# Optimization experiments

Measured on AMD Instinct MI355X. Metric: run time of the kernel, lower is better.

The kernel has to match this reference:

```python
import jax, jax.numpy as jnp
import numpy as np

EMB = 128
HEADS = 8
B = 8
T = 2048


def setup_inputs() -> dict:
    key = jax.random.key(0)
    ks = jax.random.split(key, 6)
    x = jax.random.normal(ks[0], (B, T, EMB), dtype=jnp.float32)
    # torch Linear(emb, heads*emb, bias=False): store as (in, out) so y = x @ W
    scale = 1.0 / np.sqrt(EMB)
    Wq = jax.random.uniform(ks[1], (EMB, HEADS * EMB), jnp.float32, -scale, scale)
    Wk = jax.random.uniform(ks[2], (EMB, HEADS * EMB), jnp.float32, -scale, scale)
    Wv = jax.random.uniform(ks[3], (EMB, HEADS * EMB), jnp.float32, -scale, scale)
    so = 1.0 / np.sqrt(HEADS * EMB)
    Wo = jax.random.uniform(ks[4], (HEADS * EMB, EMB), jnp.float32, -so, so)
    bo = jax.random.uniform(ks[5], (EMB,), jnp.float32, -so, so)
    return {"x": x, "Wq": Wq, "Wk": Wk, "Wv": Wv, "Wo": Wo, "bo": bo}


def reference(x, Wq, Wk, Wv, Wo, bo):
    b, t, e = x.shape
    h = HEADS
    q = (x @ Wq).reshape(b, t, h, e)  # [b,t,h,e]
    k = (x @ Wk).reshape(b, t, h, e)
    v = (x @ Wv).reshape(b, t, h, e)
    # scores: [b,h,q,k], scaled by sqrt(e) (per-head dim == emb here)
    scores = jnp.einsum('bqhe,bkhe->bhqk', q, k) / jnp.sqrt(jnp.asarray(e, x.dtype))
    attn = jax.nn.softmax(scores, axis=-1)
    out = jnp.einsum('bhqk,bkhe->bqhe', attn, v).reshape(b, t, h * e)
    return out @ Wo + bo
```

## Files before the change

### kernel.cpp

```cpp
#include <hip/hip_runtime.h>

using bf16x8 = __attribute__((ext_vector_type(8))) short;
using f32x4  = __attribute__((ext_vector_type(4))) float;

__device__ __forceinline__ ushort f2bf(float f) {
    union { float f; unsigned int u; } c; c.f = f;
    unsigned int u = c.u;
    u = (u + 0x7fffu + ((u >> 16) & 1u)) >> 16;
    return (ushort)u;
}

__device__ __forceinline__ void dma16(const ushort* g, ushort* l) {
    __builtin_amdgcn_global_load_lds(
        (const __attribute__((address_space(1))) unsigned int*)g,
        (__attribute__((address_space(3))) unsigned int*)l, 16, 0, 0);
}

constexpr int BB   = 8;
constexpr int HH   = 8;
constexpr int TT   = 2048;
constexpr int DD   = 128;
#define C2F (0.08838834764831845f * 1.4426950408889634f)

__global__ void prep_kernel(const float* __restrict__ x,
                            const float* __restrict__ Wq, const float* __restrict__ Wk,
                            const float* __restrict__ Wv, const float* __restrict__ Wo,
                            ushort* __restrict__ xb, ushort* __restrict__ WqkvT,
                            ushort* __restrict__ WoT) {
    int t = blockIdx.x * 256 + threadIdx.x;
    if (t < 524288) {
        float4 v = ((const float4*)x)[t];
        ushort4 o;
        o.x = f2bf(v.x); o.y = f2bf(v.y); o.z = f2bf(v.z); o.w = f2bf(v.w);
        ((ushort4*)xb)[t] = o;
    } else if (t < 524288 + 393216) {
        int i = t - 524288;
        int j = i >> 7, kk = i & 127;
        const float* W = (j < 1024) ? Wq : ((j < 2048) ? Wk : Wv);
        int jj = j & 1023;
        WqkvT[j * 128 + kk] = f2bf(W[kk * 1024 + jj]);
    } else {
        int i = t - 917504;
        int e = i >> 10, kk = i & 1023;
        WoT[e * 1024 + kk] = f2bf(Wo[kk * 128 + e]);
    }
}

__global__ __launch_bounds__(256, 2)
void qkv_gemm(const ushort* __restrict__ xb, const ushort* __restrict__ WqkvT,
              ushort* __restrict__ q, ushort* __restrict__ k, ushort* __restrict__ vt) {
    __shared__ ushort Al[128 * 136];
    __shared__ ushort Bl[128 * 136];
    const int tid = threadIdx.x;
    const int n0 = blockIdx.x * 128, m0 = blockIdx.y * 128;

    for (int s = tid; s < 2048; s += 256) {
        int row = s >> 4, oct = s & 15;
        *(uint4*)&Al[row * 136 + oct * 8] = *(const uint4*)&xb[m0 * 128 + s * 8];
        *(uint4*)&Bl[row * 136 + oct * 8] = *(const uint4*)&WqkvT[n0 * 128 + s * 8];
    }
    __syncthreads();

    const int w = tid >> 6, lane = tid & 63, l15 = lane & 15, g = lane >> 4;
    const int wm = (w & 1) * 64, wn = (w >> 1) * 64;
    f32x4 acc[4][4] = {};

#pragma unroll
    for (int ks = 0; ks < 4; ks++) {
        bf16x8 af[4], bfr[4];
#pragma unroll
        for (int mb = 0; mb < 4; mb++)
            af[mb] = *(const bf16x8*)&Al[(wm + mb * 16 + l15) * 136 + ks * 32 + g * 8];
#pragma unroll
        for (int nb = 0; nb < 4; nb++)
            bfr[nb] = *(const bf16x8*)&Bl[(wn + nb * 16 + l15) * 136 + ks * 32 + g * 8];
#pragma unroll
        for (int mb = 0; mb < 4; mb++)
#pragma unroll
            for (int nb = 0; nb < 4; nb++)
                acc[mb][nb] = __builtin_amdgcn_mfma_f32_16x16x32_bf16(af[mb], bfr[nb], acc[mb][nb], 0, 0, 0);
    }

    const int which = n0 >> 10;
    const int b = m0 >> 11;
    const int h = (n0 >> 7) & 7;
    const int bh = b * HH + h;
    if (which == 0) {
#pragma unroll
        for (int mb = 0; mb < 4; mb++)
#pragma unroll
            for (int nb = 0; nb < 4; nb++)
#pragma unroll
                for (int r = 0; r < 4; r++) {
                    int t = (m0 + wm + mb * 16 + g * 4 + r) & 2047;
                    int e = wn + nb * 16 + l15;
                    q[((size_t)bh * TT + t) * DD + e] = f2bf(acc[mb][nb][r]);
                }
    } else if (which == 1) {
#pragma unroll
        for (int mb = 0; mb < 4; mb++)
#pragma unroll
            for (int nb = 0; nb < 4; nb++)
#pragma unroll
                for (int r = 0; r < 4; r++) {
                    int t = (m0 + wm + mb * 16 + g * 4 + r) & 2047;
                    int e = wn + nb * 16 + l15;
                    int esw = ((((e >> 3) ^ (t & 7)) << 3) | (e & 7));
                    k[((size_t)bh * TT + t) * DD + esw] = f2bf(acc[mb][nb][r]);
                }
    } else {
        __syncthreads();
        ushort* Tl = Al;
#pragma unroll
        for (int mb = 0; mb < 4; mb++)
#pragma unroll
            for (int nb = 0; nb < 4; nb++)
#pragma unroll
                for (int r = 0; r < 4; r++)
                    Tl[(wn + nb * 16 + l15) * 136 + wm + mb * 16 + g * 4 + r] = f2bf(acc[mb][nb][r]);
        __syncthreads();
        const int c0 = (m0 & 2047) >> 6;
        for (int s = tid; s < 2048; s += 256) {
            int e = s >> 4, x = s & 15;
            int c = c0 + (x >> 3), pos = x & 7;
            int tsrc = ((pos ^ (e & 7)) * 8) + (x >> 3) * 64;
            uint4 val = *(const uint4*)&Tl[e * 136 + tsrc];
            *(uint4*)&vt[(size_t)(((bh * 32 + c) * 128) + e) * 64 + pos * 8] = val;
        }
    }
}

__global__ __launch_bounds__(256, 2)
void attn_kernel(const ushort* __restrict__ q, const ushort* __restrict__ k,
                 const ushort* __restrict__ vt, ushort* __restrict__ ao) {
    __shared__ ushort Kl[2][64 * 128];
    __shared__ ushort Vl[2][128 * 64];
    __shared__ ushort Pl[4 * 32 * 64];

    const int idx = blockIdx.x;
    const int qt128 = idx & 15, h = (idx >> 4) & 7, b = idx >> 7;
    const int t0 = qt128 * 128;
    const int bh = b * HH + h;
    const ushort* qg  = q  + (size_t)bh * TT * DD;
    const ushort* kg  = k  + (size_t)bh * TT * DD;
    const ushort* vtg = vt + (size_t)bh * 32 * DD * 64;

    const int tid = threadIdx.x, w = tid >> 6, lane = tid & 63;
    const int l15 = lane & 15, g = lane >> 4;
    const int sw = l15 & 7;

    bf16x8 qf[2][4];
#pragma unroll
    for (int qt = 0; qt < 2; qt++)
#pragma unroll
        for (int ks = 0; ks < 4; ks++)
            qf[qt][ks] = *(const bf16x8*)&qg[(size_t)(t0 + w * 32 + qt * 16 + l15) * DD + ks * 32 + g * 8];

    {
        const int seg0 = w * 2048 + lane * 8;
#pragma unroll
        for (int i = 0; i < 4; i++) {
            int seg = seg0 + i * 512;
            dma16(kg  + seg, &Kl[0][seg]);
            dma16(vtg + seg, &Vl[0][seg]);
        }
    }

    f32x4 o[2][8] = {};
    float ls[2] = {0.0f, 0.0f};

    for (int c = 0; c < 32; c++) {
        const int cur = c & 1;
        __syncthreads();

        if (c < 31) {
            const ushort* kn = kg  + (size_t)(c + 1) * 8192;
            const ushort* vn = vtg + (size_t)(c + 1) * 8192;
            const int seg0 = w * 2048 + lane * 8;
#pragma unroll
            for (int i = 0; i < 4; i++) {
                int seg = seg0 + i * 512;
                dma16(kn + seg, &Kl[cur ^ 1][seg]);
                dma16(vn + seg, &Vl[cur ^ 1][seg]);
            }
        }

        f32x4 st[4][2] = {};
#pragma unroll
        for (int kt = 0; kt < 4; kt++)
#pragma unroll
            for (int ks = 0; ks < 4; ks++) {
                bf16x8 kf = *(const bf16x8*)&Kl[cur][(kt * 16 + l15) * 128 + (((ks * 4 + g) ^ sw) * 8)];
                st[kt][0] = __builtin_amdgcn_mfma_f32_16x16x32_bf16(kf, qf[0][ks], st[kt][0], 0, 0, 0);
                st[kt][1] = __builtin_amdgcn_mfma_f32_16x16x32_bf16(kf, qf[1][ks], st[kt][1], 0, 0, 0);
            }

#pragma unroll
        for (int qt = 0; qt < 2; qt++) {
            float ps = 0.0f;
#pragma unroll
            for (int kt = 0; kt < 4; kt++) {
                ushort4 pk;
                float p0 = __builtin_amdgcn_exp2f(st[kt][qt][0] * C2F);
                float p1 = __builtin_amdgcn_exp2f(st[kt][qt][1] * C2F);
                float p2 = __builtin_amdgcn_exp2f(st[kt][qt][2] * C2F);
                float p3 = __builtin_amdgcn_exp2f(st[kt][qt][3] * C2F);
                ps += (p0 + p1) + (p2 + p3);
                pk.x = f2bf(p0); pk.y = f2bf(p1); pk.z = f2bf(p2); pk.w = f2bf(p3);
                int kb = 2 * kt + (g >> 1);
                *(ushort4*)&Pl[w * 2048 + (qt * 16 + l15) * 64 + ((kb ^ sw) * 8) + (g & 1) * 4] = pk;
            }
            ls[qt] += ps;
        }

#pragma unroll
        for (int ns = 0; ns < 2; ns++) {
            int rb = ((ns * 4 + g) ^ sw) * 8;
            bf16x8 pa0 = *(const bf16x8*)&Pl[w * 2048 + (l15) * 64 + rb];
            bf16x8 pa1 = *(const bf16x8*)&Pl[w * 2048 + (16 + l15) * 64 + rb];
#pragma unroll
            for (int eb = 0; eb < 8; eb++) {
                bf16x8 vb = *(const bf16x8*)&Vl[cur][(eb * 16 + l15) * 64 + rb];
                o[0][eb] = __builtin_amdgcn_mfma_f32_16x16x32_bf16(pa0, vb, o[0][eb], 0, 0, 0);
                o[1][eb] = __builtin_amdgcn_mfma_f32_16x16x32_bf16(pa1, vb, o[1][eb], 0, 0, 0);
            }
        }
    }

#pragma unroll
    for (int qt = 0; qt < 2; qt++) {
        float tot = ls[qt];
        tot += __shfl_xor(tot, 16);
        tot += __shfl_xor(tot, 32);
        float inv[4];
#pragma unroll
        for (int r = 0; r < 4; r++)
            inv[r] = 1.0f / __shfl(tot, g * 4 + r, 64);
#pragma unroll
        for (int eb = 0; eb < 8; eb++)
#pragma unroll
            for (int r = 0; r < 4; r++) {
                int m = t0 + w * 32 + qt * 16 + g * 4 + r;
                int col = h * 128 + eb * 16 + l15;
                ao[(size_t)(b * TT + m) * 1024 + col] = f2bf(o[qt][eb][r] * inv[r]);
            }
    }
}

__global__ __launch_bounds__(256, 2)
void outproj_gemm(const ushort* __restrict__ ao, const ushort* __restrict__ WoT,
                  const float* __restrict__ bo, float* __restrict__ out) {
    __shared__ ushort Al[64 * 72];
    __shared__ ushort Bl[64 * 72];
    const int tid = threadIdx.x;
    const int n0 = blockIdx.x * 64, m0 = blockIdx.y * 64;
    const int w = tid >> 6, lane = tid & 63, l15 = lane & 15, g = lane >> 4;
    const int wm = (w & 1) * 32, wn = (w >> 1) * 32;
    f32x4 acc[2][2] = {};

    for (int kc = 0; kc < 16; kc++) {
        int k0 = kc * 64;
        __syncthreads();
        for (int s = tid; s < 512; s += 256) {
            int row = s >> 3, oct = s & 7;
            *(uint4*)&Al[row * 72 + oct * 8] = *(const uint4*)&ao[(size_t)(m0 + row) * 1024 + k0 + oct * 8];
            *(uint4*)&Bl[row * 72 + oct * 8] = *(const uint4*)&WoT[(n0 + row) * 1024 + k0 + oct * 8];
        }
        __syncthreads();
#pragma unroll
        for (int ks = 0; ks < 2; ks++) {
            bf16x8 af[2], bfr[2];
#pragma unroll
            for (int mb = 0; mb < 2; mb++)
                af[mb] = *(const bf16x8*)&Al[(wm + mb * 16 + l15) * 72 + ks * 32 + g * 8];
#pragma unroll
            for (int nb = 0; nb < 2; nb++)
                bfr[nb] = *(const bf16x8*)&Bl[(wn + nb * 16 + l15) * 72 + ks * 32 + g * 8];
#pragma unroll
            for (int mb = 0; mb < 2; mb++)
#pragma unroll
                for (int nb = 0; nb < 2; nb++)
                    acc[mb][nb] = __builtin_amdgcn_mfma_f32_16x16x32_bf16(af[mb], bfr[nb], acc[mb][nb], 0, 0, 0);
        }
    }

#pragma unroll
    for (int mb = 0; mb < 2; mb++)
#pragma unroll
        for (int nb = 0; nb < 2; nb++) {
            int j = n0 + wn + nb * 16 + l15;
            float bias = bo[j];
#pragma unroll
            for (int r = 0; r < 4; r++) {
                int m = m0 + wm + mb * 16 + g * 4 + r;
                out[(size_t)m * 128 + j] = acc[mb][nb][r] + bias;
            }
        }
}

extern "C" void kernel_launch(void* const* d_in, const int* in_sizes, int n_in,
                              void* d_out, int out_size, void* d_ws, size_t ws_size,
                              hipStream_t stream) {
    const float* x  = (const float*)d_in[0];
    const float* Wq = (const float*)d_in[1];
    const float* Wk = (const float*)d_in[2];
    const float* Wv = (const float*)d_in[3];
    const float* Wo = (const float*)d_in[4];
    const float* bo = (const float*)d_in[5];
    float* out = (float*)d_out;

    char* ws = (char*)d_ws;
    ushort* xb    = (ushort*)(ws);
    ushort* WqkvT = (ushort*)(ws + 4194304);
    ushort* WoT   = (ushort*)(ws + 4980736);
    ushort* qb    = (ushort*)(ws + 5242880);
    ushort* kb    = (ushort*)(ws + 38797312);
    ushort* vtb   = (ushort*)(ws + 72351744);
    ushort* ao    = (ushort*)(ws + 105906176);

    prep_kernel<<<4096, 256, 0, stream>>>(x, Wq, Wk, Wv, Wo, xb, WqkvT, WoT);
    qkv_gemm<<<dim3(24, 128), 256, 0, stream>>>(xb, WqkvT, qb, kb, vtb);
    attn_kernel<<<1024, 256, 0, stream>>>(qb, kb, vtb, ao);
    outproj_gemm<<<dim3(2, 256), 256, 0, stream>>>(ao, WoT, bo, out);
}
```

Measured before the change: 279.7 us.

## Enlarge attention query tile to 256 and shrink KV chunk to 32

Attention blocks now cover 256 queries (64 per wave) instead of 128, and K/V chunks shrink from 64 to 32 keys. The V-transpose layout and its swizzle in the QKV GEMM are changed to match. Each K/V fragment loaded from LDS now feeds four query tiles, which halves K/V global and LDS traffic per query and cuts shared memory use. P-to-bf16 conversion uses a packed hardware convert when the compiler provides it. The costs are higher register pressure from 4x8 accumulators, twice as many loop iterations and barriers, and only 512 blocks to spread across the CUs.

```diff
diff --git a/kernel.cpp b/kernel.cpp
--- a/kernel.cpp
+++ b/kernel.cpp
@@ -8,6 +8,22 @@
     unsigned int u = c.u;
     u = (u + 0x7fffu + ((u >> 16) & 1u)) >> 16;
     return (ushort)u;
+}
+
+#if defined(__has_builtin)
+#if __has_builtin(__builtin_amdgcn_cvt_pk_bf16_f32)
+#define HAS_PK_BF16 1
+#endif
+#endif
+__device__ __forceinline__ unsigned int pkbf(float a, float b) {
+#ifdef HAS_PK_BF16
+    typedef __bf16 bf2 __attribute__((ext_vector_type(2)));
+    union { bf2 v; unsigned int u; } cv;
+    cv.v = __builtin_amdgcn_cvt_pk_bf16_f32(a, b);
+    return cv.u;
+#else
+    return (unsigned int)f2bf(a) | ((unsigned int)f2bf(b) << 16);
+#endif
 }
 
 __device__ __forceinline__ void dma16(const ushort* g, ushort* l) {
@@ -119,13 +135,15 @@
                 for (int r = 0; r < 4; r++)
                     Tl[(wn + nb * 16 + l15) * 136 + wm + mb * 16 + g * 4 + r] = f2bf(acc[mb][nb][r]);
         __syncthreads();
-        const int c0 = (m0 & 2047) >> 6;
+        const int c0 = (m0 & 2047) >> 5;
         for (int s = tid; s < 2048; s += 256) {
             int e = s >> 4, x = s & 15;
-            int c = c0 + (x >> 3), pos = x & 7;
-            int tsrc = ((pos ^ (e & 7)) * 8) + (x >> 3) * 64;
+            int cl = x >> 2, pos = x & 3;
+            int el = e & 15;
+            int vsw = (el ^ (el >> 2)) & 3;
+            int tsrc = cl * 32 + ((pos ^ vsw) * 8);
             uint4 val = *(const uint4*)&Tl[e * 136 + tsrc];
-            *(uint4*)&vt[(size_t)(((bh * 32 + c) * 128) + e) * 64 + pos * 8] = val;
+            *(uint4*)&vt[(size_t)(((bh * 64 + c0 + cl) * 128) + e) * 32 + pos * 8] = val;
         }
     }
 }
@@ -133,102 +151,96 @@
 __global__ __launch_bounds__(256, 2)
 void attn_kernel(const ushort* __restrict__ q, const ushort* __restrict__ k,
                  const ushort* __restrict__ vt, ushort* __restrict__ ao) {
-    __shared__ ushort Kl[2][64 * 128];
-    __shared__ ushort Vl[2][128 * 64];
-    __shared__ ushort Pl[4 * 32 * 64];
+    __shared__ ushort Kl[2][32 * 128];
+    __shared__ ushort Vl[2][128 * 32];
+    __shared__ ushort Pl[4 * 64 * 32];
 
     const int idx = blockIdx.x;
-    const int qt128 = idx & 15, h = (idx >> 4) & 7, b = idx >> 7;
-    const int t0 = qt128 * 128;
+    const int qt256 = idx & 7, h = (idx >> 3) & 7, b = idx >> 6;
+    const int t0 = qt256 * 256;
     const int bh = b * HH + h;
     const ushort* qg  = q  + (size_t)bh * TT * DD;
     const ushort* kg  = k  + (size_t)bh * TT * DD;
-    const ushort* vtg = vt + (size_t)bh * 32 * DD * 64;
+    const ushort* vtg = vt + (size_t)bh * 64 * DD * 32;
 
     const int tid = threadIdx.x, w = tid >> 6, lane = tid & 63;
     const int l15 = lane & 15, g = lane >> 4;
-    const int sw = l15 & 7;
-
-    bf16x8 qf[2][4];
-#pragma unroll
-    for (int qt = 0; qt < 2; qt++)
+    const int swk = l15 & 7;
+    const int swv = (l15 ^ (l15 >> 2)) & 3;
+
+    bf16x8 qf[4][4];
+#pragma unroll
+    for (int qt = 0; qt < 4; qt++)
 #pragma unroll
         for (int ks = 0; ks < 4; ks++)
-            qf[qt][ks] = *(const bf16x8*)&qg[(size_t)(t0 + w * 32 + qt * 16 + l15) * DD + ks * 32 + g * 8];
-
-    {
-        const int seg0 = w * 2048 + lane * 8;
-#pragma unroll
-        for (int i = 0; i < 4; i++) {
-            int seg = seg0 + i * 512;
-            dma16(kg  + seg, &Kl[0][seg]);
-            dma16(vtg + seg, &Vl[0][seg]);
-        }
-    }
-
-    f32x4 o[2][8] = {};
-    float ls[2] = {0.0f, 0.0f};
-
-    for (int c = 0; c < 32; c++) {
+            qf[qt][ks] = *(const bf16x8*)&qg[(size_t)(t0 + w * 64 + qt * 16 + l15) * DD + ks * 32 + g * 8];
+
+    const int seg = tid * 8;
+#pragma unroll
+    for (int j = 0; j < 2; j++) {
+        dma16(kg  + seg + j * 2048, &Kl[0][seg + j * 2048]);
+        dma16(vtg + seg + j * 2048, &Vl[0][seg + j * 2048]);
+    }
+
+    f32x4 o[4][8] = {};
+    float ls[4] = {0.0f, 0.0f, 0.0f, 0.0f};
+
+    for (int c = 0; c < 64; c++) {
         const int cur = c & 1;
         __syncthreads();
 
-        if (c < 31) {
-            const ushort* kn = kg  + (size_t)(c + 1) * 8192;
-            const ushort* vn = vtg + (size_t)(c + 1) * 8192;
-            const int seg0 = w * 2048 + lane * 8;
-#pragma unroll
-            for (int i = 0; i < 4; i++) {
-                int seg = seg0 + i * 512;
-                dma16(kn + seg, &Kl[cur ^ 1][seg]);
-                dma16(vn + seg, &Vl[cur ^ 1][seg]);
-            }
-        }
-
-        f32x4 st[4][2] = {};
-#pragma unroll
-        for (int kt = 0; kt < 4; kt++)
+        if (c < 63) {
+            const ushort* kn = kg  + (size_t)(c + 1) * 4096;
+            const ushort* vn = vtg + (size_t)(c + 1) * 4096;
+#pragma unroll
+            for (int j = 0; j < 2; j++) {
+                dma16(kn + seg + j * 2048, &Kl[cur ^ 1][seg + j * 2048]);
+                dma16(vn + seg + j * 2048, &Vl[cur ^ 1][seg + j * 2048]);
+            }
+        }
+
+#pragma unroll
+        for (int kt = 0; kt < 2; kt++) {
+            f32x4 st[4] = {};
 #pragma unroll
             for (int ks = 0; ks < 4; ks++) {
-                bf16x8 kf = *(const bf16x8*)&Kl[cur][(kt * 16 + l15) * 128 + (((ks * 4 + g) ^ sw) * 8)];
-                st[kt][0] = __builtin_amdgcn_mfma_f32_16x16x32_bf16(kf, qf[0][ks], st[kt][0], 0, 0, 0);
-                st[kt][1] = __builtin_amdgcn_mfma_f32_16x16x32_bf16(kf, qf[1][ks], st[kt][1], 0, 0, 0);
-            }
-
-#pragma unroll
-        for (int qt = 0; qt < 2; qt++) {
-            float ps = 0.0f;
-#pragma unroll
-            for (int kt = 0; kt < 4; kt++) {
-                ushort4 pk;
-                float p0 = __builtin_amdgcn_exp2f(st[kt][qt][0] * C2F);
-                float p1 = __builtin_amdgcn_exp2f(st[kt][qt][1] * C2F);
-                float p2 = __builtin_amdgcn_exp2f(st[kt][qt][2] * C2F);
-                float p3 = __builtin_amdgcn_exp2f(st[kt][qt][3] * C2F);
-                ps += (p0 + p1) + (p2 + p3);
-                pk.x = f2bf(p0); pk.y = f2bf(p1); pk.z = f2bf(p2); pk.w = f2bf(p3);
-                int kb = 2 * kt + (g >> 1);
-                *(ushort4*)&Pl[w * 2048 + (qt * 16 + l15) * 64 + ((kb ^ sw) * 8) + (g & 1) * 4] = pk;
-            }
-            ls[qt] += ps;
-        }
-
-#pragma unroll
-        for (int ns = 0; ns < 2; ns++) {
-            int rb = ((ns * 4 + g) ^ sw) * 8;
-            bf16x8 pa0 = *(const bf16x8*)&Pl[w * 2048 + (l15) * 64 + rb];
-            bf16x8 pa1 = *(const bf16x8*)&Pl[w * 2048 + (16 + l15) * 64 + rb];
+                bf16x8 kf = *(const bf16x8*)&Kl[cur][(kt * 16 + l15) * 128 + (((ks * 4 + g) ^ swk) * 8)];
+#pragma unroll
+                for (int qt = 0; qt < 4; qt++)
+                    st[qt] = __builtin_amdgcn_mfma_f32_16x16x32_bf16(kf, qf[qt][ks], st[qt], 0, 0, 0);
+            }
+            const int kb = 2 * kt + (g >> 1);
+#pragma unroll
+            for (int qt = 0; qt < 4; qt++) {
+                float p0 = __builtin_amdgcn_exp2f(st[qt][0] * C2F);
+                float p1 = __builtin_amdgcn_exp2f(st[qt][1] * C2F);
+                float p2 = __builtin_amdgcn_exp2f(st[qt][2] * C2F);
+                float p3 = __builtin_amdgcn_exp2f(st[qt][3] * C2F);
+                ls[qt] += (p0 + p1) + (p2 + p3);
+                uint2 pk;
+                pk.x = pkbf(p0, p1);
+                pk.y = pkbf(p2, p3);
+                *(uint2*)&Pl[w * 2048 + (qt * 16 + l15) * 32 + ((kb ^ swv) * 8) + (g & 1) * 4] = pk;
+            }
+        }
+
+        {
+            bf16x8 pa[4];
+#pragma unroll
+            for (int qt = 0; qt < 4; qt++)
+                pa[qt] = *(const bf16x8*)&Pl[w * 2048 + (qt * 16 + l15) * 32 + ((g ^ swv) * 8)];
 #pragma unroll
             for (int eb = 0; eb < 8; eb++) {
-                bf16x8 vb = *(const bf16x8*)&Vl[cur][(eb * 16 + l15) * 64 + rb];
-                o[0][eb] = __builtin_amdgcn_mfma_f32_16x16x32_bf16(pa0, vb, o[0][eb], 0, 0, 0);
-                o[1][eb] = __builtin_amdgcn_mfma_f32_16x16x32_bf16(pa1, vb, o[1][eb], 0, 0, 0);
-            }
-        }
-    }
-
-#pragma unroll
-    for (int qt = 0; qt < 2; qt++) {
+                bf16x8 vb = *(const bf16x8*)&Vl[cur][(eb * 16 + l15) * 32 + ((g ^ swv) * 8)];
+#pragma unroll
+                for (int qt = 0; qt < 4; qt++)
+                    o[qt][eb] = __builtin_amdgcn_mfma_f32_16x16x32_bf16(pa[qt], vb, o[qt][eb], 0, 0, 0);
+            }
+        }
+    }
+
+#pragma unroll
+    for (int qt = 0; qt < 4; qt++) {
         float tot = ls[qt];
         tot += __shfl_xor(tot, 16);
         tot += __shfl_xor(tot, 32);
@@ -240,7 +252,7 @@
         for (int eb = 0; eb < 8; eb++)
 #pragma unroll
             for (int r = 0; r < 4; r++) {
-                int m = t0 + w * 32 + qt * 16 + g * 4 + r;
+                int m = t0 + w * 64 + qt * 16 + g * 4 + r;
                 int col = h * 128 + eb * 16 + l15;
                 ao[(size_t)(b * TT + m) * 1024 + col] = f2bf(o[qt][eb][r] * inv[r]);
             }
@@ -320,6 +332,6 @@
 
     prep_kernel<<<4096, 256, 0, stream>>>(x, Wq, Wk, Wv, Wo, xb, WqkvT, WoT);
     qkv_gemm<<<dim3(24, 128), 256, 0, stream>>>(xb, WqkvT, qb, kb, vtb);
-    attn_kernel<<<1024, 256, 0, stream>>>(qb, kb, vtb, ao);
+    attn_kernel<<<512, 256, 0, stream>>>(qb, kb, vtb, ao);
     outproj_gemm<<<dim3(2, 256), 256, 0, stream>>>(ao, WoT, bo, out);
 }
```

After: 275.0 us. About the same (-1.7%).
